# Performance work log

Measured on AMD Instinct MI355X. Metric: run time of the kernel, lower is better.

The kernel has to match this reference:

```python
import jax, jax.numpy as jnp
import numpy as np

MARGIN = 0.2
EPS = 1e-12  # F.normalize eps


def _l2norm(x, axis):
    n = jnp.linalg.norm(x, axis=axis, keepdims=True)
    return x / jnp.maximum(n, EPS)


def setup_inputs() -> dict:
    key = jax.random.key(0)
    k1, k2, k3, k4 = jax.random.split(key, 4)
    B, L_im, L_s, D = 256, 37, 33, 1024
    im_set = jax.random.normal(k1, (B, L_im, D), dtype=jnp.float32)
    s_seq = jax.random.normal(k2, (B, L_s, D), dtype=jnp.float32)
    # realistic valid lengths (>= a few regions/words, <= max)
    im_len = jax.random.randint(k3, (B,), 10, L_im + 1, dtype=jnp.int32)
    s_len = jax.random.randint(k4, (B,), 8, L_s + 1, dtype=jnp.int32)
    return {"im_set": im_set, "s_seq": s_seq, "im_len": im_len, "s_len": s_len}


def _aggr_similarity(im_set, s_seq, im_len, s_len):
    # l2-normalize feature dim, then drop CLS region / special tokens
    im = _l2norm(im_set, axis=2)[:, 1:, :]          # [B, Li, D]
    s = _l2norm(s_seq, axis=2)[:, 1:-2, :]          # [B, Ls, D]
    im_l = im_len - 1
    s_l = s_len - 3
    Li, Ls = im.shape[1], s.shape[1]
    # cross-batch alignment scores: [B_im, B_s, Li, Ls]
    align = jnp.einsum('bid,cjd->bcij', im, s)
    im_invalid = jnp.arange(Li)[None, :] >= im_l[:, None]   # [B, Li]
    s_invalid = jnp.arange(Ls)[None, :] >= s_l[:, None]     # [B, Ls]
    mask = im_invalid[:, None, :, None] | s_invalid[None, :, None, :]
    align = jnp.where(mask, 0.0, align)
    # 'MrSw': max over image regions, sum over sentence words
    return align.max(axis=2).sum(axis=2)             # [B_im, B_s]


def _contrastive_loss(scores):
    B = scores.shape[0]
    diag = jnp.diagonal(scores)                      # [B]
    cost_s = jnp.maximum(MARGIN + scores - diag[:, None], 0.0)
    cost_im = jnp.maximum(MARGIN + scores - diag[None, :], 0.0)
    eye = jnp.eye(B, dtype=bool)
    cost_s = jnp.where(eye, 0.0, cost_s)
    cost_im = jnp.where(eye, 0.0, cost_im)
    # max_violation=True: hardest negatives
    return cost_s.max(axis=1).sum() + cost_im.max(axis=0).sum()


def reference(im_set, s_seq, im_len, s_len):
    scores = _aggr_similarity(im_set, s_seq, im_len, s_len)
    return _contrastive_loss(scores)
```

## Files before the change

### kernel.cpp

```cpp
#include <hip/hip_runtime.h>
#include <hip/hip_bf16.h>


typedef __attribute__((ext_vector_type(8))) short bf16x8;
typedef __attribute__((ext_vector_type(4))) float f32x4;

#define NB   256
#define DIM  1024
#define LI   36
#define LIP  36
#define LS   30
#define LSP  32

static __device__ inline ushort f2bf(float x) {
    union { __hip_bfloat16 h; ushort u; } cvt;
    cvt.h = __float2bfloat16(x);
    return cvt.u;
}

static __device__ __forceinline__ void gload_lds16(const void* g, void* l) {
    __builtin_amdgcn_global_load_lds(
        (const __attribute__((address_space(1))) void*)g,
        (__attribute__((address_space(3))) void*)l, 16, 0, 0);
}

__global__ __launch_bounds__(256) void normalize_pack(
    const float* __restrict__ im, const float* __restrict__ sq,
    short* __restrict__ imp, short* __restrict__ sp)
{
    const int gw   = (blockIdx.x * 256 + threadIdx.x) >> 6;
    const int lane = threadIdx.x & 63;
    const int NIM  = NB * LI;

    const float* src = nullptr;
    short* dst;
    if (gw < NIM) {
        int b = gw / LI, i = gw - b * LI;
        dst = imp + (size_t)gw * DIM;
        src = im + ((size_t)b * 37 + i + 1) * DIM;
    } else {
        int g2 = gw - NIM;
        int b = g2 >> 5, j = g2 & 31;
        dst = sp + (size_t)g2 * DIM;
        if (j < LS) src = sq + ((size_t)b * 33 + j + 1) * DIM;
    }

    if (src) {
        const float4* s4 = (const float4*)src;
        float4 v[4];
        float ss = 0.f;
        #pragma unroll
        for (int t = 0; t < 4; ++t) {
            float4 x = s4[lane + 64 * t];
            v[t] = x;
            ss += x.x * x.x + x.y * x.y + x.z * x.z + x.w * x.w;
        }
        #pragma unroll
        for (int o = 32; o >= 1; o >>= 1) ss += __shfl_xor(ss, o, 64);
        float scale = 1.0f / fmaxf(sqrtf(ss), 1e-12f);
        ushort4* d4 = (ushort4*)dst;
        #pragma unroll
        for (int t = 0; t < 4; ++t) {
            float4 x = v[t];
            ushort4 o;
            o.x = f2bf(x.x * scale);
            o.y = f2bf(x.y * scale);
            o.z = f2bf(x.z * scale);
            o.w = f2bf(x.w * scale);
            d4[lane + 64 * t] = o;
        }
    } else {
        uint4 z = {0u, 0u, 0u, 0u};
        uint4* d4 = (uint4*)dst;
        d4[lane] = z;
        d4[lane + 64] = z;
    }
}

__global__ __launch_bounds__(256, 2) void gemm_scores(
    const short* __restrict__ imp, const short* __restrict__ sp,
    const int* __restrict__ im_len, const int* __restrict__ s_len,
    float* __restrict__ scores)
{
    __shared__ short As[144 * 64];
    __shared__ short Bs[256 * 64];

    const int tid  = threadIdx.x;
    const int wave = tid >> 6;
    const int lane = tid & 63;
    const int q    = lane >> 4;
    const int l15  = lane & 15;
    const int b0   = blockIdx.x * 4;
    const int c0   = blockIdx.y * 8;

    f32x4 acc[9][4];
    #pragma unroll
    for (int mt = 0; mt < 9; ++mt)
        #pragma unroll
        for (int t = 0; t < 4; ++t)
            acc[mt][t] = (f32x4){0.f, 0.f, 0.f, 0.f};

    const int srow   = lane >> 3;
    const int schunk = (lane & 7) ^ srow;
    const char* gA = (const char*)imp + (size_t)(b0 * LIP) * 2048
                     + srow * 2048 + schunk * 16;
    const char* gB = (const char*)sp + (size_t)(c0 * LSP) * 2048
                     + srow * 2048 + schunk * 16;

    const int cs0 = ((q)     ^ (l15 & 7)) * 16;
    const int cs1 = ((4 + q) ^ (l15 & 7)) * 16;

    const int wa4 = wave * 4;
    const int wb8 = wave * 8;

    for (int k0 = 0; k0 < DIM; k0 += 64) {
        const int kb = k0 * 2;
        #pragma unroll
        for (int it = 0; it < 4; ++it) {
            const int rb = wa4 + it;
            gload_lds16(gA + rb * (8 * 2048) + kb, (char*)As + rb * 1024);
        }
        if (wave < 2) {
            const int rb = 16 + wave;
            gload_lds16(gA + rb * (8 * 2048) + kb, (char*)As + rb * 1024);
        }
        #pragma unroll
        for (int it = 0; it < 8; ++it) {
            const int rb = wb8 + it;
            gload_lds16(gB + rb * (8 * 2048) + kb, (char*)Bs + rb * 1024);
        }
        __syncthreads();
        #pragma unroll
        for (int g = 0; g < 2; ++g) {
            const int cs = g ? cs1 : cs0;
            bf16x8 af[9], bfr[4];
            #pragma unroll
            for (int mt = 0; mt < 9; ++mt)
                af[mt] = *(const bf16x8*)((const char*)As + (mt * 16 + l15) * 128 + cs);
            #pragma unroll
            for (int t = 0; t < 4; ++t)
                bfr[t] = *(const bf16x8*)((const char*)Bs + ((wave * 4 + t) * 16 + l15) * 128 + cs);
            #pragma unroll
            for (int mt = 0; mt < 9; ++mt)
                #pragma unroll
                for (int t = 0; t < 4; ++t)
                    acc[mt][t] = __builtin_amdgcn_mfma_f32_16x16x32_bf16(
                        af[mt], bfr[t], acc[mt][t], 0, 0, 0);
        }
        __syncthreads();
    }

    int il[4];
    #pragma unroll
    for (int bb = 0; bb < 4; ++bb) il[bb] = im_len[b0 + bb] - 1;

    float sc[4][2] = {{0.f,0.f},{0.f,0.f},{0.f,0.f},{0.f,0.f}};
    #pragma unroll
    for (int t = 0; t < 4; ++t) {
        const int nt = wave * 4 + t;
        const int c  = c0 + (nt >> 1);
        const int sl = s_len[c] - 3;
        const int jj = (nt & 1) * 16 + l15;
        const bool jv = (jj < sl);

        float m[4] = {-3.4e38f, -3.4e38f, -3.4e38f, -3.4e38f};
        #pragma unroll
        for (int mt = 0; mt < 9; ++mt) {
            const int im_lo = (4 * mt) / 9;
            const int im_hi = (4 * mt + 3) / 9;
            const int thr   = 9 * im_hi - 4 * mt;
            #pragma unroll
            for (int r = 0; r < 4; ++r) {
                const float v = acc[mt][t][r];
                const int base = mt * 16 + q * 4 + r;
                if (im_lo == im_hi) {
                    const int i = base - 36 * im_lo;
                    if (i < il[im_lo]) m[im_lo] = fmaxf(m[im_lo], v);
                } else {
                    const bool hi = (q >= thr);
                    if (!hi) {
                        const int i = base - 36 * im_lo;
                        if (i < il[im_lo]) m[im_lo] = fmaxf(m[im_lo], v);
                    } else {
                        const int i = base - 36 * im_hi;
                        if (i < il[im_hi]) m[im_hi] = fmaxf(m[im_hi], v);
                    }
                }
            }
        }
        #pragma unroll
        for (int bb = 0; bb < 4; ++bb) {
            float mm = m[bb];
            mm = fmaxf(mm, __shfl_xor(mm, 16, 64));
            mm = fmaxf(mm, __shfl_xor(mm, 32, 64));
            if (il[bb] < LI) mm = fmaxf(mm, 0.f);
            float v = (q == 0 && jv) ? mm : 0.f;
            #pragma unroll
            for (int off = 32; off >= 1; off >>= 1) v += __shfl_xor(v, off, 64);
            sc[bb][t >> 1] += v;
        }
    }
    if (lane == 0) {
        #pragma unroll
        for (int bb = 0; bb < 4; ++bb)
            #pragma unroll
            for (int h = 0; h < 2; ++h)
                scores[(b0 + bb) * NB + c0 + wave * 2 + h] = sc[bb][h];
    }
}

__global__ __launch_bounds__(256) void loss_fused(
    const float* __restrict__ sc, float* __restrict__ out)
{
    const int wave = threadIdx.x >> 6, lane = threadIdx.x & 63;
    const int t = blockIdx.x * 4 + wave;
    const float dt = sc[t * (NB + 1)];
    float rowmax = 0.f, colmax = 0.f;
    #pragma unroll
    for (int p = 0; p < 4; ++p) {
        const int k = lane + 64 * p;
        const float r = sc[t * NB + k];
        const float c = sc[k * NB + t];
        if (k != t) {
            rowmax = fmaxf(rowmax, 0.2f + r - dt);
            colmax = fmaxf(colmax, 0.2f + c - dt);
        }
    }
    #pragma unroll
    for (int o = 32; o >= 1; o >>= 1) {
        rowmax = fmaxf(rowmax, __shfl_xor(rowmax, o, 64));
        colmax = fmaxf(colmax, __shfl_xor(colmax, o, 64));
    }
    __shared__ float red[4];
    if (lane == 0) red[wave] = fmaxf(rowmax, 0.f) + fmaxf(colmax, 0.f);
    __syncthreads();
    if (threadIdx.x == 0)
        atomicAdd(out, red[0] + red[1] + red[2] + red[3]);
}

extern "C" void kernel_launch(void* const* d_in, const int* in_sizes, int n_in,
                              void* d_out, int out_size, void* d_ws, size_t ws_size,
                              hipStream_t stream) {
    const float* im_set = (const float*)d_in[0];
    const float* s_seq  = (const float*)d_in[1];
    const int*   im_len = (const int*)d_in[2];
    const int*   s_len  = (const int*)d_in[3];
    float* out = (float*)d_out;

    char* ws = (char*)d_ws;
    const size_t imp_bytes = (size_t)NB * LIP * DIM * 2;
    const size_t sp_bytes  = (size_t)NB * LSP * DIM * 2;
    short* imp    = (short*)ws;
    short* sp     = (short*)(ws + imp_bytes);
    float* scores = (float*)(ws + imp_bytes + sp_bytes);

    normalize_pack<<<4352, 256, 0, stream>>>(im_set, s_seq, imp, sp);

    dim3 grid(NB / 4, NB / 8);
    gemm_scores<<<grid, 256, 0, stream>>>(imp, sp, im_len, s_len, scores);

    loss_fused<<<64, 256, 0, stream>>>(scores, out);
}
```

Before: 242.8 us.

## Triple-buffer GEMM K-loop with async LDS prefetch two slices ahead

After: 306.9 us. 1.26x slower.

```diff
diff --git a/kernel.cpp b/kernel.cpp
--- a/kernel.cpp
+++ b/kernel.cpp
@@ -11,6 +11,16 @@
 #define LIP  36
 #define LS   30
 #define LSP  32
+#define ABYTES 9216
+#define BUFB   25600
+#define NSLICE 32
+
+#define PIPE_SYNC(N) do { \
+    __builtin_amdgcn_sched_barrier(0); \
+    asm volatile("s_waitcnt vmcnt(" #N ")" ::: "memory"); \
+    __builtin_amdgcn_s_barrier(); \
+    __builtin_amdgcn_sched_barrier(0); \
+} while (0)
 
 static __device__ inline ushort f2bf(float x) {
     union { __hip_bfloat16 h; ushort u; } cvt;
@@ -82,8 +92,7 @@
     const int* __restrict__ im_len, const int* __restrict__ s_len,
     float* __restrict__ scores)
 {
-    __shared__ short As[144 * 64];
-    __shared__ short Bs[256 * 64];
+    __shared__ __align__(1024) char lds[3 * BUFB];
 
     const int tid  = threadIdx.x;
     const int wave = tid >> 6;
@@ -100,55 +109,69 @@
         for (int t = 0; t < 4; ++t)
             acc[mt][t] = (f32x4){0.f, 0.f, 0.f, 0.f};
 
-    const int srow   = lane >> 3;
-    const int schunk = (lane & 7) ^ srow;
-    const char* gA = (const char*)imp + (size_t)(b0 * LIP) * 2048
-                     + srow * 2048 + schunk * 16;
-    const char* gB = (const char*)sp + (size_t)(c0 * LSP) * 2048
-                     + srow * 2048 + schunk * 16;
-
-    const int cs0 = ((q)     ^ (l15 & 7)) * 16;
-    const int cs1 = ((4 + q) ^ (l15 & 7)) * 16;
-
-    const int wa4 = wave * 4;
-    const int wb8 = wave * 8;
-
-    for (int k0 = 0; k0 < DIM; k0 += 64) {
-        const int kb = k0 * 2;
-        #pragma unroll
-        for (int it = 0; it < 4; ++it) {
-            const int rb = wa4 + it;
-            gload_lds16(gA + rb * (8 * 2048) + kb, (char*)As + rb * 1024);
-        }
-        if (wave < 2) {
-            const int rb = 16 + wave;
-            gload_lds16(gA + rb * (8 * 2048) + kb, (char*)As + rb * 1024);
-        }
-        #pragma unroll
-        for (int it = 0; it < 8; ++it) {
-            const int rb = wb8 + it;
-            gload_lds16(gB + rb * (8 * 2048) + kb, (char*)Bs + rb * 1024);
-        }
-        __syncthreads();
-        #pragma unroll
-        for (int g = 0; g < 2; ++g) {
-            const int cs = g ? cs1 : cs0;
-            bf16x8 af[9], bfr[4];
-            #pragma unroll
-            for (int mt = 0; mt < 9; ++mt)
-                af[mt] = *(const bf16x8*)((const char*)As + (mt * 16 + l15) * 128 + cs);
+    const int i8 = lane >> 3;
+    const int ph = lane & 7;
+    const int sl = ph ^ i8;
+    const int off_lane = (2 * i8 + (sl >> 2)) * 2048 + (sl & 3) * 16;
+
+    const char* baseA = (const char*)imp + (size_t)(b0 * LIP) * 2048;
+    const char* baseB = (const char*)sp  + (size_t)(c0 * LSP) * 2048;
+
+    const char* g7[7];
+    int l7[7];
+    #pragma unroll
+    for (int j = 0; j < 7; ++j) {
+        const int cid = wave + 4 * j;
+        if (cid < 9) {
+            g7[j] = baseA + cid * (16 * 2048) + off_lane;
+            l7[j] = cid * 1024;
+        } else {
+            const int bc = (cid < 25 ? cid : 9) - 9;
+            g7[j] = baseB + bc * (16 * 2048) + off_lane;
+            l7[j] = ABYTES + bc * 1024;
+        }
+    }
+    const int nst = (wave == 0) ? 7 : 6;
+
+    const int cs2 = (((l15 & 1) * 4 + q) ^ ((l15 >> 1) & 7)) * 16;
+    const int lhalf = l15 >> 1;
+
+    auto compute = [&](const char* buf) {
+        bf16x8 af[9], bfr[4];
+        #pragma unroll
+        for (int mt = 0; mt < 9; ++mt)
+            af[mt] = *(const bf16x8*)(buf + (8 * mt + lhalf) * 128 + cs2);
+        #pragma unroll
+        for (int t = 0; t < 4; ++t)
+            bfr[t] = *(const bf16x8*)(buf + ABYTES + (8 * (wave * 4 + t) + lhalf) * 128 + cs2);
+        __builtin_amdgcn_s_setprio(1);
+        #pragma unroll
+        for (int mt = 0; mt < 9; ++mt)
             #pragma unroll
             for (int t = 0; t < 4; ++t)
-                bfr[t] = *(const bf16x8*)((const char*)Bs + ((wave * 4 + t) * 16 + l15) * 128 + cs);
-            #pragma unroll
-            for (int mt = 0; mt < 9; ++mt)
-                #pragma unroll
-                for (int t = 0; t < 4; ++t)
-                    acc[mt][t] = __builtin_amdgcn_mfma_f32_16x16x32_bf16(
-                        af[mt], bfr[t], acc[mt][t], 0, 0, 0);
-        }
-        __syncthreads();
-    }
+                acc[mt][t] = __builtin_amdgcn_mfma_f32_16x16x32_bf16(
+                    af[mt], bfr[t], acc[mt][t], 0, 0, 0);
+        __builtin_amdgcn_s_setprio(0);
+    };
+
+    for (int j = 0; j < nst; ++j) gload_lds16(g7[j], lds + l7[j]);
+    for (int j = 0; j < nst; ++j) gload_lds16(g7[j] + 64, lds + BUFB + l7[j]);
+
+    int cur = 0;
+    #pragma unroll 1
+    for (int kk = 0; kk < NSLICE - 2; ++kk) {
+        PIPE_SYNC(6);
+        const int nb = (cur + 2 >= 3) ? cur - 1 : cur + 2;
+        for (int j = 0; j < nst; ++j)
+            gload_lds16(g7[j] + (kk + 2) * 64, lds + nb * BUFB + l7[j]);
+        compute(lds + cur * BUFB);
+        cur = (cur == 2) ? 0 : cur + 1;
+    }
+    PIPE_SYNC(6);
+    compute(lds + cur * BUFB);
+    cur = (cur == 2) ? 0 : cur + 1;
+    PIPE_SYNC(0);
+    compute(lds + cur * BUFB);
 
     int il[4];
     #pragma unroll
@@ -159,9 +182,9 @@
     for (int t = 0; t < 4; ++t) {
         const int nt = wave * 4 + t;
         const int c  = c0 + (nt >> 1);
-        const int sl = s_len[c] - 3;
+        const int sl2 = s_len[c] - 3;
         const int jj = (nt & 1) * 16 + l15;
-        const bool jv = (jj < sl);
+        const bool jv = (jj < sl2);
 
         float m[4] = {-3.4e38f, -3.4e38f, -3.4e38f, -3.4e38f};
         #pragma unroll
```
